# Performance work log

Hardware: AMD Instinct MI355X
Metric: run time of the kernel (lower is better)

The kernel has to match this reference:

```python
import jax, jax.numpy as jnp
import numpy as np

CONTEXT_SIZE = 32
NDIM = 64
HEAD_SIZE = 64
BATCH = 16384


def setup_inputs() -> dict:
    key = jax.random.key(0)
    kx, kk, kq, kv = jax.random.split(key, 4)
    x = jax.random.normal(kx, (BATCH, CONTEXT_SIZE, NDIM), dtype=jnp.float32)
    # nn.Linear(ndim, head_size, bias=False): y = x @ W.T, W is [head_size, ndim].
    # We store transposed weights [ndim, head_size] so y = x @ W.
    scale = 1.0 / np.sqrt(NDIM)
    Wk = jax.random.normal(kk, (NDIM, HEAD_SIZE), dtype=jnp.float32) * scale
    Wq = jax.random.normal(kq, (NDIM, HEAD_SIZE), dtype=jnp.float32) * scale
    Wv = jax.random.normal(kv, (NDIM, HEAD_SIZE), dtype=jnp.float32) * scale
    return {"x": x, "Wk": Wk, "Wq": Wq, "Wv": Wv}


def reference(x, Wk, Wq, Wv):
    # x: [B, T, D] with T == CONTEXT_SIZE
    k = x @ Wk  # [B, T, H]
    q = x @ Wq  # [B, T, H]
    v = x @ Wv  # [B, T, H]
    # Faithful to source: p = q @ k^T / head_size**(-0.5) == q @ k^T * sqrt(head_size)
    p = jnp.einsum("bth,bsh->bts", q, k) * jnp.sqrt(jnp.float32(HEAD_SIZE))
    causal = jnp.tril(jnp.ones((CONTEXT_SIZE, CONTEXT_SIZE), dtype=bool))
    p = jnp.where(causal, p, -jnp.inf)
    p = jax.nn.softmax(p, axis=-1)
    # dropout is identity in eval mode
    return jnp.einsum("bts,bsh->bth", p, v)  # [B, T, H]
```

## Files before the change

kernel.cpp:

```cpp
#include <hip/hip_runtime.h>

typedef __attribute__((ext_vector_type(8))) short short8;
typedef __attribute__((ext_vector_type(4))) float f32x4;

#define CTX 32
#define ND  64
#define NH  64
#define LOG2E_8 11.541560327111707f

#define OFF_MH 0
#define OFF_ML 8192
#define OFF_WV 16384
#define OFF_WAVE 24576
#define PWSTR 80
#define PW_RTH 0
#define PW_RTL 2560
#define PW_VT  0
#define PW_P   5120
#define WAVE_BYTES 7168
#define LDS_BYTES (OFF_WAVE + 4 * WAVE_BYTES)

__device__ __forceinline__ unsigned short f2bf(float f) {
  unsigned int u = __builtin_bit_cast(unsigned int, f);
  u += 0x7FFFu + ((u >> 16) & 1u);
  return (unsigned short)(u >> 16);
}
__device__ __forceinline__ float bf2f(unsigned short b) {
  unsigned int u = ((unsigned int)b) << 16;
  return __builtin_bit_cast(float, u);
}

#define MFMA(a, b, c) __builtin_amdgcn_mfma_f32_16x16x32_bf16((a), (b), (c), 0, 0, 0)

__global__ __launch_bounds__(256) void mk_m(
    const float* __restrict__ Wq, const float* __restrict__ Wk,
    unsigned short* __restrict__ MtH, unsigned short* __restrict__ MtL)
{
  const int idx = blockIdx.x * 256 + threadIdx.x;
  const int dp = idx >> 6, d = idx & 63;
  const float* wq = Wq + d * 64;
  const float* wk = Wk + dp * 64;
  float acc = 0.f;
  #pragma unroll
  for (int h = 0; h < 64; ++h) acc = fmaf(wq[h], wk[h], acc);
  acc *= LOG2E_8;
  const unsigned short hi = f2bf(acc);
  MtH[idx] = hi;
  MtL[idx] = f2bf(acc - bf2f(hi));
}

__global__ __launch_bounds__(256, 3) void head_fused(
    const float* __restrict__ x, const float* __restrict__ Wv,
    const unsigned short* __restrict__ MtH_g, const unsigned short* __restrict__ MtL_g,
    float* __restrict__ out)
{
  __shared__ __align__(16) char lds[LDS_BYTES];
  const int tid = threadIdx.x;

  {
    const unsigned int* srcH = (const unsigned int*)MtH_g;
    const unsigned int* srcL = (const unsigned int*)MtL_g;
    #pragma unroll
    for (int i = 0; i < 8; ++i) {
      const int e = tid + 256 * i;
      const int row = e >> 5;
      const int byte = row * 128 + (((e & 31) * 4) ^ ((row & 7) << 4));
      *(unsigned int*)(lds + OFF_MH + byte) = srcH[e];
      *(unsigned int*)(lds + OFF_ML + byte) = srcL[e];
    }
    #pragma unroll
    for (int i = 0; i < 16; ++i) {
      const int e = tid + 256 * i;
      const int d = e >> 6, h = e & 63;
      const int byte = h * 128 + ((2 * d) ^ ((h & 7) << 4));
      *(unsigned short*)(lds + OFF_WV + byte) = f2bf(Wv[e]);
    }
  }
  __syncthreads();

  const int wid  = tid >> 6;
  const int lane = tid & 63;
  const int c = lane & 15;
  const int g = lane >> 4;
  char* const wl = lds + OFF_WAVE + wid * WAVE_BYTES;

  const long b = (long)blockIdx.x * 4 + wid;
  const float* const xb = x + b * (CTX * ND);

  short8 xh[2][2], xl[2][2];
  #pragma unroll
  for (int mt = 0; mt < 2; ++mt) {
    #pragma unroll
    for (int kt = 0; kt < 2; ++kt) {
      const float* p = xb + (16 * mt + c) * ND + 32 * kt + 8 * g;
      const f32x4 a0 = *(const f32x4*)(p);
      const f32x4 a1 = *(const f32x4*)(p + 4);
      short8 hi, lo;
      #pragma unroll
      for (int j = 0; j < 4; ++j) {
        const unsigned short h0 = f2bf(a0[j]);
        hi[j] = (short)h0;
        lo[j] = (short)f2bf(a0[j] - bf2f(h0));
        const unsigned short h1 = f2bf(a1[j]);
        hi[4 + j] = (short)h1;
        lo[4 + j] = (short)f2bf(a1[j] - bf2f(h1));
      }
      xh[mt][kt] = hi;
      xl[mt][kt] = lo;
    }
  }

  f32x4 pa[2][2] = {{{0.f,0.f,0.f,0.f},{0.f,0.f,0.f,0.f}},
                    {{0.f,0.f,0.f,0.f},{0.f,0.f,0.f,0.f}}};
  #pragma unroll
  for (int kt = 0; kt < 2; ++kt) {
    #pragma unroll
    for (int ntl = 0; ntl < 2; ++ntl) {
      const int nt = 2 * kt + ntl;
      f32x4 a0 = {0.f, 0.f, 0.f, 0.f};
      f32x4 a1 = {0.f, 0.f, 0.f, 0.f};
      #pragma unroll
      for (int kk = 0; kk < 2; ++kk) {
        const int row = 16 * nt + c;
        const int byte = row * 128 + ((64 * kk + 16 * g) ^ ((row & 7) << 4));
        const short8 bh = *(const short8*)(lds + OFF_MH + byte);
        const short8 bl = *(const short8*)(lds + OFF_ML + byte);
        a0 = MFMA(xh[0][kk], bh, a0);
        a0 = MFMA(xh[0][kk], bl, a0);
        a0 = MFMA(xl[0][kk], bh, a0);
        a1 = MFMA(xh[1][kk], bh, a1);
        a1 = MFMA(xh[1][kk], bl, a1);
        a1 = MFMA(xl[1][kk], bh, a1);
      }
      #pragma unroll
      for (int j = 0; j < 4; ++j) {
        const int col2 = 2 * (16 * ntl + c);
        const int off0 = (4 * g + j) * PWSTR + col2;
        const int off1 = (16 + 4 * g + j) * PWSTR + col2;
        const unsigned short h0 = f2bf(a0[j]);
        *(unsigned short*)(wl + PW_RTH + off0) = h0;
        *(unsigned short*)(wl + PW_RTL + off0) = f2bf(a0[j] - bf2f(h0));
        const unsigned short h1 = f2bf(a1[j]);
        *(unsigned short*)(wl + PW_RTH + off1) = h1;
        *(unsigned short*)(wl + PW_RTL + off1) = f2bf(a1[j] - bf2f(h1));
      }
    }
    short8 tH[2], tL[2];
    #pragma unroll
    for (int i = 0; i < 2; ++i) {
      const int off = (16 * i + c) * PWSTR + 16 * g;
      tH[i] = *(const short8*)(wl + PW_RTH + off);
      tL[i] = *(const short8*)(wl + PW_RTL + off);
    }
    #pragma unroll
    for (int mt = 0; mt < 2; ++mt) {
      #pragma unroll
      for (int nt2 = 0; nt2 < 2; ++nt2) {
        pa[mt][nt2] = MFMA(tH[mt], xh[nt2][kt], pa[mt][nt2]);
        pa[mt][nt2] = MFMA(tH[mt], xl[nt2][kt], pa[mt][nt2]);
        pa[mt][nt2] = MFMA(tL[mt], xh[nt2][kt], pa[mt][nt2]);
      }
    }
  }

  char* const pbuf = wl + PW_P;
  #pragma unroll
  for (int mt = 0; mt < 2; ++mt) {
    #pragma unroll
    for (int j = 0; j < 4; ++j) {
      const int t = 16 * mt + 4 * g + j;
      float v0 = pa[mt][0][j];
      float v1 = pa[mt][1][j];
      if (c > t)      v0 = -__builtin_inff();
      if (16 + c > t) v1 = -__builtin_inff();
      float m = fmaxf(v0, v1);
      m = fmaxf(m, __shfl_xor(m, 1));
      m = fmaxf(m, __shfl_xor(m, 2));
      m = fmaxf(m, __shfl_xor(m, 4));
      m = fmaxf(m, __shfl_xor(m, 8));
      const float e0 = exp2f(v0 - m);
      const float e1 = exp2f(v1 - m);
      float s = e0 + e1;
      s += __shfl_xor(s, 1);
      s += __shfl_xor(s, 2);
      s += __shfl_xor(s, 4);
      s += __shfl_xor(s, 8);
      const float r = 1.0f / s;
      *(unsigned short*)(pbuf + t * 64 + 2 * c)        = f2bf(e0 * r);
      *(unsigned short*)(pbuf + t * 64 + 32 + 2 * c)   = f2bf(e1 * r);
    }
  }

  #pragma unroll
  for (int nt = 0; nt < 4; ++nt) {
    f32x4 a0 = {0.f, 0.f, 0.f, 0.f};
    f32x4 a1 = {0.f, 0.f, 0.f, 0.f};
    #pragma unroll
    for (int kk = 0; kk < 2; ++kk) {
      const int row = 16 * nt + c;
      const int byte = row * 128 + ((64 * kk + 16 * g) ^ ((row & 7) << 4));
      const short8 bv = *(const short8*)(lds + OFF_WV + byte);
      a0 = MFMA(xh[0][kk], bv, a0);
      a1 = MFMA(xh[1][kk], bv, a1);
    }
    #pragma unroll
    for (int j = 0; j < 4; ++j) {
      char* const vrow = wl + PW_VT + (16 * nt + c) * PWSTR;
      *(unsigned short*)(vrow + 2 * (4 * g + j))      = f2bf(a0[j]);
      *(unsigned short*)(vrow + 2 * (16 + 4 * g + j)) = f2bf(a1[j]);
    }
  }

  const short8 ap0 = *(const short8*)(pbuf + c * 64 + 16 * g);
  const short8 ap1 = *(const short8*)(pbuf + (16 + c) * 64 + 16 * g);
  float* const ob = out + b * (CTX * NH);
  #pragma unroll
  for (int nt = 0; nt < 4; ++nt) {
    const short8 bv = *(const short8*)(wl + PW_VT + (16 * nt + c) * PWSTR + 16 * g);
    f32x4 o0 = {0.f, 0.f, 0.f, 0.f};
    f32x4 o1 = {0.f, 0.f, 0.f, 0.f};
    o0 = MFMA(ap0, bv, o0);
    o1 = MFMA(ap1, bv, o1);
    #pragma unroll
    for (int j = 0; j < 4; ++j) {
      ob[(4 * g + j) * NH + 16 * nt + c]      = o0[j];
      ob[(16 + 4 * g + j) * NH + 16 * nt + c] = o1[j];
    }
  }
}

extern "C" void kernel_launch(void* const* d_in, const int* in_sizes, int n_in,
                              void* d_out, int out_size, void* d_ws, size_t ws_size,
                              hipStream_t stream) {
  const float* x  = (const float*)d_in[0];
  const float* Wk = (const float*)d_in[1];
  const float* Wq = (const float*)d_in[2];
  const float* Wv = (const float*)d_in[3];
  float* out = (float*)d_out;

  unsigned short* MtH = (unsigned short*)d_ws;
  unsigned short* MtL = MtH + 64 * 64;

  mk_m<<<dim3(16), dim3(256), 0, stream>>>(Wq, Wk, MtH, MtL);

  const int batch = in_sizes[0] / (CTX * ND);
  head_fused<<<dim3(batch / 4), dim3(256), 0, stream>>>(x, Wv, MtH, MtL, out);
}
```

Baseline: 65.86 us.

## Read precomputed weight matrices from global/L2 instead of staging them in LDS

Converts and transposes Wv to bf16 in the prep kernel and removes the per-block LDS staging of the Mt hi/lo and Wv tiles, along with its __syncthreads. The fused kernel now loads B fragments directly from global memory and relies on cache hits. LDS per block shrinks from 53 KB to 28 KB and the launch bound is raised to 5 blocks per CU to increase occupancy. The trade is more global and L1 load traffic per wave and register pressure under the tighter launch bound.

```diff
diff --git a/kernel.cpp b/kernel.cpp
--- a/kernel.cpp
+++ b/kernel.cpp
@@ -8,17 +8,13 @@
 #define NH  64
 #define LOG2E_8 11.541560327111707f
 
-#define OFF_MH 0
-#define OFF_ML 8192
-#define OFF_WV 16384
-#define OFF_WAVE 24576
 #define PWSTR 80
 #define PW_RTH 0
 #define PW_RTL 2560
 #define PW_VT  0
 #define PW_P   5120
 #define WAVE_BYTES 7168
-#define LDS_BYTES (OFF_WAVE + 4 * WAVE_BYTES)
+#define LDS_BYTES (4 * WAVE_BYTES)
 
 __device__ __forceinline__ unsigned short f2bf(float f) {
   unsigned int u = __builtin_bit_cast(unsigned int, f);
@@ -34,7 +30,9 @@
 
 __global__ __launch_bounds__(256) void mk_m(
     const float* __restrict__ Wq, const float* __restrict__ Wk,
-    unsigned short* __restrict__ MtH, unsigned short* __restrict__ MtL)
+    const float* __restrict__ Wv,
+    unsigned short* __restrict__ MtH, unsigned short* __restrict__ MtL,
+    unsigned short* __restrict__ WvT)
 {
   const int idx = blockIdx.x * 256 + threadIdx.x;
   const int dp = idx >> 6, d = idx & 63;
@@ -47,42 +45,23 @@
   const unsigned short hi = f2bf(acc);
   MtH[idx] = hi;
   MtL[idx] = f2bf(acc - bf2f(hi));
-}
-
-__global__ __launch_bounds__(256, 3) void head_fused(
-    const float* __restrict__ x, const float* __restrict__ Wv,
-    const unsigned short* __restrict__ MtH_g, const unsigned short* __restrict__ MtL_g,
+  WvT[idx] = f2bf(Wv[d * 64 + dp]);
+}
+
+__global__ __launch_bounds__(256, 5) void head_fused(
+    const float* __restrict__ x,
+    const unsigned short* __restrict__ MtH, const unsigned short* __restrict__ MtL,
+    const unsigned short* __restrict__ WvT,
     float* __restrict__ out)
 {
   __shared__ __align__(16) char lds[LDS_BYTES];
   const int tid = threadIdx.x;
 
-  {
-    const unsigned int* srcH = (const unsigned int*)MtH_g;
-    const unsigned int* srcL = (const unsigned int*)MtL_g;
-    #pragma unroll
-    for (int i = 0; i < 8; ++i) {
-      const int e = tid + 256 * i;
-      const int row = e >> 5;
-      const int byte = row * 128 + (((e & 31) * 4) ^ ((row & 7) << 4));
-      *(unsigned int*)(lds + OFF_MH + byte) = srcH[e];
-      *(unsigned int*)(lds + OFF_ML + byte) = srcL[e];
-    }
-    #pragma unroll
-    for (int i = 0; i < 16; ++i) {
-      const int e = tid + 256 * i;
-      const int d = e >> 6, h = e & 63;
-      const int byte = h * 128 + ((2 * d) ^ ((h & 7) << 4));
-      *(unsigned short*)(lds + OFF_WV + byte) = f2bf(Wv[e]);
-    }
-  }
-  __syncthreads();
-
   const int wid  = tid >> 6;
   const int lane = tid & 63;
   const int c = lane & 15;
   const int g = lane >> 4;
-  char* const wl = lds + OFF_WAVE + wid * WAVE_BYTES;
+  char* const wl = lds + wid * WAVE_BYTES;
 
   const long b = (long)blockIdx.x * 4 + wid;
   const float* const xb = x + b * (CTX * ND);
@@ -121,10 +100,9 @@
       f32x4 a1 = {0.f, 0.f, 0.f, 0.f};
       #pragma unroll
       for (int kk = 0; kk < 2; ++kk) {
-        const int row = 16 * nt + c;
-        const int byte = row * 128 + ((64 * kk + 16 * g) ^ ((row & 7) << 4));
-        const short8 bh = *(const short8*)(lds + OFF_MH + byte);
-        const short8 bl = *(const short8*)(lds + OFF_ML + byte);
+        const int eoff = (16 * nt + c) * 64 + 32 * kk + 8 * g;
+        const short8 bh = *(const short8*)(MtH + eoff);
+        const short8 bl = *(const short8*)(MtL + eoff);
         a0 = MFMA(xh[0][kk], bh, a0);
         a0 = MFMA(xh[0][kk], bl, a0);
         a0 = MFMA(xl[0][kk], bh, a0);
@@ -197,9 +175,8 @@
     f32x4 a1 = {0.f, 0.f, 0.f, 0.f};
     #pragma unroll
     for (int kk = 0; kk < 2; ++kk) {
-      const int row = 16 * nt + c;
-      const int byte = row * 128 + ((64 * kk + 16 * g) ^ ((row & 7) << 4));
-      const short8 bv = *(const short8*)(lds + OFF_WV + byte);
+      const int eoff = (16 * nt + c) * 64 + 32 * kk + 8 * g;
+      const short8 bv = *(const short8*)(WvT + eoff);
       a0 = MFMA(xh[0][kk], bv, a0);
       a1 = MFMA(xh[1][kk], bv, a1);
     }
@@ -240,9 +217,10 @@
 
   unsigned short* MtH = (unsigned short*)d_ws;
   unsigned short* MtL = MtH + 64 * 64;
-
-  mk_m<<<dim3(16), dim3(256), 0, stream>>>(Wq, Wk, MtH, MtL);
+  unsigned short* WvT = MtL + 64 * 64;
+
+  mk_m<<<dim3(16), dim3(256), 0, stream>>>(Wq, Wk, Wv, MtH, MtL, WvT);
 
   const int batch = in_sizes[0] / (CTX * ND);
-  head_fused<<<dim3(batch / 4), dim3(256), 0, stream>>>(x, Wv, MtH, MtL, out);
-}
+  head_fused<<<dim3(batch / 4), dim3(256), 0, stream>>>(x, MtH, MtL, WvT, out);
+}
```

Result: slower. 90.29 us (+37.1%).

## Process two batches per wave with prefetched x and transposed softmax layout

Applied to the files above, without the earlier changes.

Each wave now handles two batch elements and prefetches the next element's x into registers while computing the current one, which halves the grid and amortizes the per-block LDS weight setup. Wv is transposed and converted to bf16 in the pre-kernel, so the main kernel fills LDS with simple 32-bit copies. The QK MFMA operands are swapped so softmax rows reduce with two cross-group shuffles, and the P, V and output stores become vectorized packed writes. The cost is higher register pressure from the prefetch buffers and fewer blocks to hide latency.

```diff
diff --git a/kernel.cpp b/kernel.cpp
--- a/kernel.cpp
+++ b/kernel.cpp
@@ -2,11 +2,13 @@
 
 typedef __attribute__((ext_vector_type(8))) short short8;
 typedef __attribute__((ext_vector_type(4))) float f32x4;
+typedef __attribute__((ext_vector_type(2))) unsigned int u32x2;
 
 #define CTX 32
 #define ND  64
 #define NH  64
 #define LOG2E_8 11.541560327111707f
+#define NB_PER_WAVE 2
 
 #define OFF_MH 0
 #define OFF_ML 8192
@@ -29,12 +31,17 @@
   unsigned int u = ((unsigned int)b) << 16;
   return __builtin_bit_cast(float, u);
 }
+__device__ __forceinline__ unsigned int pk2(float a, float b) {
+  return (unsigned int)f2bf(a) | ((unsigned int)f2bf(b) << 16);
+}
 
 #define MFMA(a, b, c) __builtin_amdgcn_mfma_f32_16x16x32_bf16((a), (b), (c), 0, 0, 0)
 
 __global__ __launch_bounds__(256) void mk_m(
     const float* __restrict__ Wq, const float* __restrict__ Wk,
-    unsigned short* __restrict__ MtH, unsigned short* __restrict__ MtL)
+    const float* __restrict__ Wv,
+    unsigned short* __restrict__ MtH, unsigned short* __restrict__ MtL,
+    unsigned short* __restrict__ WvT)
 {
   const int idx = blockIdx.x * 256 + threadIdx.x;
   const int dp = idx >> 6, d = idx & 63;
@@ -47,63 +54,40 @@
   const unsigned short hi = f2bf(acc);
   MtH[idx] = hi;
   MtL[idx] = f2bf(acc - bf2f(hi));
-}
-
-__global__ __launch_bounds__(256, 3) void head_fused(
-    const float* __restrict__ x, const float* __restrict__ Wv,
-    const unsigned short* __restrict__ MtH_g, const unsigned short* __restrict__ MtL_g,
-    float* __restrict__ out)
-{
-  __shared__ __align__(16) char lds[LDS_BYTES];
-  const int tid = threadIdx.x;
-
-  {
-    const unsigned int* srcH = (const unsigned int*)MtH_g;
-    const unsigned int* srcL = (const unsigned int*)MtL_g;
-    #pragma unroll
-    for (int i = 0; i < 8; ++i) {
-      const int e = tid + 256 * i;
-      const int row = e >> 5;
-      const int byte = row * 128 + (((e & 31) * 4) ^ ((row & 7) << 4));
-      *(unsigned int*)(lds + OFF_MH + byte) = srcH[e];
-      *(unsigned int*)(lds + OFF_ML + byte) = srcL[e];
-    }
-    #pragma unroll
-    for (int i = 0; i < 16; ++i) {
-      const int e = tid + 256 * i;
-      const int d = e >> 6, h = e & 63;
-      const int byte = h * 128 + ((2 * d) ^ ((h & 7) << 4));
-      *(unsigned short*)(lds + OFF_WV + byte) = f2bf(Wv[e]);
-    }
-  }
-  __syncthreads();
-
-  const int wid  = tid >> 6;
-  const int lane = tid & 63;
-  const int c = lane & 15;
-  const int g = lane >> 4;
-  char* const wl = lds + OFF_WAVE + wid * WAVE_BYTES;
-
-  const long b = (long)blockIdx.x * 4 + wid;
-  const float* const xb = x + b * (CTX * ND);
-
-  short8 xh[2][2], xl[2][2];
-  #pragma unroll
-  for (int mt = 0; mt < 2; ++mt) {
+  WvT[idx] = f2bf(Wv[d * 64 + dp]);
+}
+
+__device__ __forceinline__ void load_x(const float* __restrict__ xb,
+                                       f32x4 (&xr)[2][2][2], int c, int g) {
+  #pragma unroll
+  for (int mt = 0; mt < 2; ++mt)
     #pragma unroll
     for (int kt = 0; kt < 2; ++kt) {
       const float* p = xb + (16 * mt + c) * ND + 32 * kt + 8 * g;
-      const f32x4 a0 = *(const f32x4*)(p);
-      const f32x4 a1 = *(const f32x4*)(p + 4);
+      xr[mt][kt][0] = *(const f32x4*)(p);
+      xr[mt][kt][1] = *(const f32x4*)(p + 4);
+    }
+}
+
+__device__ __forceinline__ void compute_batch(
+    const f32x4 (&xr)[2][2][2], char* lds, char* wl,
+    float* __restrict__ ob, int c, int g)
+{
+  short8 xh[2][2], xl[2][2];
+  #pragma unroll
+  for (int mt = 0; mt < 2; ++mt) {
+    #pragma unroll
+    for (int kt = 0; kt < 2; ++kt) {
       short8 hi, lo;
       #pragma unroll
-      for (int j = 0; j < 4; ++j) {
-        const unsigned short h0 = f2bf(a0[j]);
-        hi[j] = (short)h0;
-        lo[j] = (short)f2bf(a0[j] - bf2f(h0));
-        const unsigned short h1 = f2bf(a1[j]);
-        hi[4 + j] = (short)h1;
-        lo[4 + j] = (short)f2bf(a1[j] - bf2f(h1));
+      for (int half = 0; half < 2; ++half) {
+        #pragma unroll
+        for (int j = 0; j < 4; ++j) {
+          const float f = xr[mt][kt][half][j];
+          const unsigned short h = f2bf(f);
+          hi[4 * half + j] = (short)h;
+          lo[4 * half + j] = (short)f2bf(f - bf2f(h));
+        }
       }
       xh[mt][kt] = hi;
       xl[mt][kt] = lo;
@@ -156,38 +140,40 @@
     for (int mt = 0; mt < 2; ++mt) {
       #pragma unroll
       for (int nt2 = 0; nt2 < 2; ++nt2) {
-        pa[mt][nt2] = MFMA(tH[mt], xh[nt2][kt], pa[mt][nt2]);
-        pa[mt][nt2] = MFMA(tH[mt], xl[nt2][kt], pa[mt][nt2]);
-        pa[mt][nt2] = MFMA(tL[mt], xh[nt2][kt], pa[mt][nt2]);
+        pa[mt][nt2] = MFMA(xh[mt][kt], tH[nt2], pa[mt][nt2]);
+        pa[mt][nt2] = MFMA(xl[mt][kt], tH[nt2], pa[mt][nt2]);
+        pa[mt][nt2] = MFMA(xh[mt][kt], tL[nt2], pa[mt][nt2]);
       }
     }
   }
 
   char* const pbuf = wl + PW_P;
   #pragma unroll
-  for (int mt = 0; mt < 2; ++mt) {
-    #pragma unroll
-    for (int j = 0; j < 4; ++j) {
-      const int t = 16 * mt + 4 * g + j;
-      float v0 = pa[mt][0][j];
-      float v1 = pa[mt][1][j];
-      if (c > t)      v0 = -__builtin_inff();
-      if (16 + c > t) v1 = -__builtin_inff();
-      float m = fmaxf(v0, v1);
-      m = fmaxf(m, __shfl_xor(m, 1));
-      m = fmaxf(m, __shfl_xor(m, 2));
-      m = fmaxf(m, __shfl_xor(m, 4));
-      m = fmaxf(m, __shfl_xor(m, 8));
-      const float e0 = exp2f(v0 - m);
-      const float e1 = exp2f(v1 - m);
-      float s = e0 + e1;
-      s += __shfl_xor(s, 1);
-      s += __shfl_xor(s, 2);
-      s += __shfl_xor(s, 4);
-      s += __shfl_xor(s, 8);
-      const float r = 1.0f / s;
-      *(unsigned short*)(pbuf + t * 64 + 2 * c)        = f2bf(e0 * r);
-      *(unsigned short*)(pbuf + t * 64 + 32 + 2 * c)   = f2bf(e1 * r);
+  for (int nt = 0; nt < 2; ++nt) {
+    const int t = 16 * nt + c;
+    float v[8];
+    #pragma unroll
+    for (int mt = 0; mt < 2; ++mt)
+      #pragma unroll
+      for (int j = 0; j < 4; ++j) {
+        const int s = 16 * mt + 4 * g + j;
+        v[4 * mt + j] = (s <= t) ? pa[mt][nt][j] : -__builtin_inff();
+      }
+    float m = fmaxf(fmaxf(fmaxf(v[0], v[1]), fmaxf(v[2], v[3])),
+                    fmaxf(fmaxf(v[4], v[5]), fmaxf(v[6], v[7])));
+    m = fmaxf(m, __shfl_xor(m, 16));
+    m = fmaxf(m, __shfl_xor(m, 32));
+    float e[8], ssum = 0.f;
+    #pragma unroll
+    for (int i = 0; i < 8; ++i) { e[i] = exp2f(v[i] - m); ssum += e[i]; }
+    ssum += __shfl_xor(ssum, 16);
+    ssum += __shfl_xor(ssum, 32);
+    const float r = __builtin_amdgcn_rcpf(ssum);
+    #pragma unroll
+    for (int mt = 0; mt < 2; ++mt) {
+      const u32x2 w2 = {pk2(e[4 * mt] * r, e[4 * mt + 1] * r),
+                        pk2(e[4 * mt + 2] * r, e[4 * mt + 3] * r)};
+      *(u32x2*)(pbuf + t * 64 + 32 * mt + 8 * g) = w2;
     }
   }
 
@@ -203,28 +189,77 @@
       a0 = MFMA(xh[0][kk], bv, a0);
       a1 = MFMA(xh[1][kk], bv, a1);
     }
-    #pragma unroll
-    for (int j = 0; j < 4; ++j) {
-      char* const vrow = wl + PW_VT + (16 * nt + c) * PWSTR;
-      *(unsigned short*)(vrow + 2 * (4 * g + j))      = f2bf(a0[j]);
-      *(unsigned short*)(vrow + 2 * (16 + 4 * g + j)) = f2bf(a1[j]);
-    }
+    char* const vrow = wl + PW_VT + (16 * nt + c) * PWSTR;
+    const u32x2 w0 = {pk2(a0[0], a0[1]), pk2(a0[2], a0[3])};
+    const u32x2 w1 = {pk2(a1[0], a1[1]), pk2(a1[2], a1[3])};
+    *(u32x2*)(vrow + 8 * g)      = w0;
+    *(u32x2*)(vrow + 32 + 8 * g) = w1;
   }
 
   const short8 ap0 = *(const short8*)(pbuf + c * 64 + 16 * g);
   const short8 ap1 = *(const short8*)(pbuf + (16 + c) * 64 + 16 * g);
-  float* const ob = out + b * (CTX * NH);
-  #pragma unroll
-  for (int nt = 0; nt < 4; ++nt) {
-    const short8 bv = *(const short8*)(wl + PW_VT + (16 * nt + c) * PWSTR + 16 * g);
+  #pragma unroll
+  for (int mh = 0; mh < 4; ++mh) {
+    const short8 bv = *(const short8*)(wl + PW_VT + (16 * mh + c) * PWSTR + 16 * g);
     f32x4 o0 = {0.f, 0.f, 0.f, 0.f};
     f32x4 o1 = {0.f, 0.f, 0.f, 0.f};
-    o0 = MFMA(ap0, bv, o0);
-    o1 = MFMA(ap1, bv, o1);
-    #pragma unroll
-    for (int j = 0; j < 4; ++j) {
-      ob[(4 * g + j) * NH + 16 * nt + c]      = o0[j];
-      ob[(16 + 4 * g + j) * NH + 16 * nt + c] = o1[j];
+    o0 = MFMA(bv, ap0, o0);
+    o1 = MFMA(bv, ap1, o1);
+    *(f32x4*)(ob + c * NH + 16 * mh + 4 * g)        = o0;
+    *(f32x4*)(ob + (16 + c) * NH + 16 * mh + 4 * g) = o1;
+  }
+}
+
+__global__ __launch_bounds__(256, 3) void head_fused(
+    const float* __restrict__ x,
+    const unsigned short* __restrict__ MtH, const unsigned short* __restrict__ MtL,
+    const unsigned short* __restrict__ WvT,
+    float* __restrict__ out, int wstride)
+{
+  __shared__ __align__(16) char lds[LDS_BYTES];
+  const int tid = threadIdx.x;
+
+  {
+    const unsigned int* srcH = (const unsigned int*)MtH;
+    const unsigned int* srcL = (const unsigned int*)MtL;
+    const unsigned int* srcV = (const unsigned int*)WvT;
+    #pragma unroll
+    for (int i = 0; i < 8; ++i) {
+      const int e = tid + 256 * i;
+      const int row = e >> 5;
+      const int byte = row * 128 + (((e & 31) * 4) ^ ((row & 7) << 4));
+      *(unsigned int*)(lds + OFF_MH + byte) = srcH[e];
+      *(unsigned int*)(lds + OFF_ML + byte) = srcL[e];
+      *(unsigned int*)(lds + OFF_WV + byte) = srcV[e];
+    }
+  }
+  __syncthreads();
+
+  const int wid  = tid >> 6;
+  const int lane = tid & 63;
+  const int c = lane & 15;
+  const int g = lane >> 4;
+  char* const wl = lds + OFF_WAVE + wid * WAVE_BYTES;
+
+  const int w = blockIdx.x * 4 + wid;
+
+  f32x4 xc[2][2][2];
+  load_x(x + (long)w * (CTX * ND), xc, c, g);
+
+  #pragma unroll
+  for (int it = 0; it < NB_PER_WAVE; ++it) {
+    const long b = (long)w + (long)it * wstride;
+    f32x4 xn[2][2][2];
+    if (it + 1 < NB_PER_WAVE)
+      load_x(x + (b + wstride) * (CTX * ND), xn, c, g);
+    compute_batch(xc, lds, wl, out + b * (CTX * NH), c, g);
+    if (it + 1 < NB_PER_WAVE) {
+      #pragma unroll
+      for (int i = 0; i < 2; ++i)
+        #pragma unroll
+        for (int k = 0; k < 2; ++k)
+          #pragma unroll
+          for (int h = 0; h < 2; ++h) xc[i][k][h] = xn[i][k][h];
     }
   }
 }
@@ -240,9 +275,11 @@
 
   unsigned short* MtH = (unsigned short*)d_ws;
   unsigned short* MtL = MtH + 64 * 64;
-
-  mk_m<<<dim3(16), dim3(256), 0, stream>>>(Wq, Wk, MtH, MtL);
+  unsigned short* WvT = MtL + 64 * 64;
+
+  mk_m<<<dim3(16), dim3(256), 0, stream>>>(Wq, Wk, Wv, MtH, MtL, WvT);
 
   const int batch = in_sizes[0] / (CTX * ND);
-  head_fused<<<dim3(batch / 4), dim3(256), 0, stream>>>(x, Wv, MtH, MtL, out);
-}
+  const int wstride = batch / NB_PER_WAVE;
+  head_fused<<<dim3(wstride / 4), dim3(256), 0, stream>>>(x, MtH, MtL, WvT, out, wstride);
+}
```

After: 59.45 us. 9.7% less time.
